# Kernel tuning notes

Hardware: AMD Instinct MI355X
Metric: run time of the kernel (lower is better)

Reference implementation:

```python
import jax, jax.numpy as jnp
import numpy as np

N_NODES = 100000
N_EDGES = 1600000
IN_FEATS = 64
OUT_FEATS = 64
DIM = 3
N_KERNELS = 4


def setup_inputs() -> dict:
    key = jax.random.key(0)
    ks = jax.random.split(key, 8)
    feat = jax.random.normal(ks[0], (N_NODES, IN_FEATS), dtype=jnp.float32)
    pseudo = jax.random.uniform(ks[1], (N_EDGES, DIM), dtype=jnp.float32)
    src = jax.random.randint(ks[2], (N_EDGES,), 0, N_NODES, dtype=jnp.int32)
    dst = jax.random.randint(ks[3], (N_EDGES,), 0, N_NODES, dtype=jnp.int32)
    W_fc = jax.random.normal(ks[4], (N_KERNELS * OUT_FEATS, IN_FEATS), dtype=jnp.float32) * 0.1
    mu = jax.random.normal(ks[5], (N_KERNELS, DIM), dtype=jnp.float32)
    inv_sigma = jax.random.uniform(ks[6], (N_KERNELS, DIM), dtype=jnp.float32) + 0.5
    bias = jnp.zeros((OUT_FEATS,), dtype=jnp.float32)
    return {"feat": feat, "pseudo": pseudo, "src": src, "dst": dst,
            "W_fc": W_fc, "mu": mu, "inv_sigma": inv_sigma, "bias": bias}


def reference(feat, pseudo, src, dst, W_fc, mu, inv_sigma, bias):
    N = feat.shape[0]
    K, out = N_KERNELS, OUT_FEATS
    # node projections: [N, K, out]
    h = (feat @ W_fc.T).reshape(N, K, out)
    # per-edge Gaussian kernel weights: [E, K]
    diff = pseudo[:, None, :] - mu[None, :, :]            # [E, K, dim]
    g = jnp.exp(jnp.sum(-0.5 * diff * diff * (inv_sigma[None] ** 2), axis=-1))
    # sum-aggregate: sum_k sum_{e: dst=v} h[src_e, k] * g[e, k]
    # (kernel sum and edge sum commute for sum reducer; loop over K avoids [E,K,out])
    rst = jnp.zeros((N, out), dtype=feat.dtype)
    for k in range(K):
        msg = h[:, k, :][src] * g[:, k:k + 1]             # [E, out]
        rst = rst + jax.ops.segment_sum(msg, dst, num_segments=N)
    # residual (Identity since in_feats == out_feats) + bias
    rst = rst + feat + bias
    return rst
```

## Files before the change

kernel.cpp:

```cpp
#include <hip/hip_runtime.h>

#define N_NODES_C 100000
#define N_EDGES_C 1600000
#define IN_F 64
#define OUT_F 64
#define NK 4
#define SCAN_BLK 256
#define NBLK ((N_NODES_C + SCAN_BLK - 1) / SCAN_BLK)
#define EBLK (N_EDGES_C / 256)
#define CPAD 16
#define NSLICE 8
#define SLICE_N (N_NODES_C / NSLICE)
#define SCAT_GRID 2048

__device__ __forceinline__ unsigned int f2bf(float x) {
    unsigned int u = __float_as_uint(x);
    return (u + 0x7fffu + ((u >> 16) & 1u)) >> 16;
}
__device__ __forceinline__ float bflo(unsigned int u) { return __uint_as_float(u << 16); }
__device__ __forceinline__ float bfhi(unsigned int u) { return __uint_as_float(u & 0xffff0000u); }

__global__ __launch_bounds__(256, 2) void proj_hist_kernel(
    const int* __restrict__ dst, int* __restrict__ cnt,
    const float* __restrict__ feat, const float* __restrict__ W,
    unsigned short* __restrict__ hb, int n_nodes)
{
    {
        const int gsz = (int)gridDim.x * 256;
        for (int e = (int)blockIdx.x * 256 + (int)threadIdx.x; e < N_EDGES_C; e += gsz)
            atomicAdd(&cnt[dst[e]], 1);
    }
    __shared__ float frow[4][IN_F];
    const int t = threadIdx.x;
    const int o = t >> 2;
    const int k = t & 3;
    float wreg[IN_F];
    {
        const float4* W4 = reinterpret_cast<const float4*>(W + (size_t)(k * OUT_F + o) * IN_F);
        #pragma unroll
        for (int i = 0; i < IN_F / 4; ++i) {
            float4 v = W4[i];
            wreg[4*i+0] = v.x; wreg[4*i+1] = v.y; wreg[4*i+2] = v.z; wreg[4*i+3] = v.w;
        }
    }
    const int nn4 = n_nodes >> 2;
    for (int q = blockIdx.x; q < nn4; q += gridDim.x) {
        const int n0 = q << 2;
        if (t < 64) {
            float4 v = reinterpret_cast<const float4*>(feat + (size_t)n0 * IN_F)[t];
            reinterpret_cast<float4*>(frow[t >> 4])[t & 15] = v;
        }
        __syncthreads();
        const float4* f0 = reinterpret_cast<const float4*>(frow[0]);
        const float4* f1 = reinterpret_cast<const float4*>(frow[1]);
        const float4* f2 = reinterpret_cast<const float4*>(frow[2]);
        const float4* f3 = reinterpret_cast<const float4*>(frow[3]);
        float a0 = 0.f, a1 = 0.f, a2 = 0.f, a3 = 0.f;
        #pragma unroll
        for (int i = 0; i < IN_F / 4; ++i) {
            const float4 v0 = f0[i], v1 = f1[i], v2 = f2[i], v3 = f3[i];
            const float w0 = wreg[4*i], w1 = wreg[4*i+1], w2 = wreg[4*i+2], w3 = wreg[4*i+3];
            a0 = fmaf(v0.x,w0, fmaf(v0.y,w1, fmaf(v0.z,w2, fmaf(v0.w,w3, a0))));
            a1 = fmaf(v1.x,w0, fmaf(v1.y,w1, fmaf(v1.z,w2, fmaf(v1.w,w3, a1))));
            a2 = fmaf(v2.x,w0, fmaf(v2.y,w1, fmaf(v2.z,w2, fmaf(v2.w,w3, a2))));
            a3 = fmaf(v3.x,w0, fmaf(v3.y,w1, fmaf(v3.z,w2, fmaf(v3.w,w3, a3))));
        }
        hb[(size_t)(n0+0) * 256 + t] = (unsigned short)f2bf(a0);
        hb[(size_t)(n0+1) * 256 + t] = (unsigned short)f2bf(a1);
        hb[(size_t)(n0+2) * 256 + t] = (unsigned short)f2bf(a2);
        hb[(size_t)(n0+3) * 256 + t] = (unsigned short)f2bf(a3);
        __syncthreads();
    }
}

__global__ __launch_bounds__(256) void scan1_kernel(
    const int* __restrict__ cnt, int* __restrict__ bsum)
{
    __shared__ int s[SCAN_BLK];
    int i = blockIdx.x * SCAN_BLK + threadIdx.x;
    int v = (i < N_NODES_C) ? cnt[i] : 0;
    s[threadIdx.x] = v; __syncthreads();
    for (int off = SCAN_BLK / 2; off > 0; off >>= 1) {
        if (threadIdx.x < off) s[threadIdx.x] += s[threadIdx.x + off];
        __syncthreads();
    }
    if (threadIdx.x == 0) bsum[blockIdx.x] = s[0];
}

__global__ __launch_bounds__(256) void scan23_kernel(
    const int* __restrict__ cnt, const int* __restrict__ bsum,
    int* __restrict__ row_start, int* __restrict__ cursor_pad)
{
    __shared__ int pre[SCAN_BLK];
    __shared__ int s[SCAN_BLK];
    const int t = threadIdx.x;
    int p = 0;
    for (int i = t; i < (int)blockIdx.x; i += SCAN_BLK) p += bsum[i];
    pre[t] = p; __syncthreads();
    for (int off = SCAN_BLK / 2; off > 0; off >>= 1) {
        if (t < off) pre[t] += pre[t + off];
        __syncthreads();
    }
    const int boff = pre[0];
    const int i = blockIdx.x * SCAN_BLK + t;
    int v = (i < N_NODES_C) ? cnt[i] : 0;
    s[t] = v; __syncthreads();
    for (int off = 1; off < SCAN_BLK; off <<= 1) {
        int x = (t >= off) ? s[t - off] : 0;
        __syncthreads();
        s[t] += x;
        __syncthreads();
    }
    if (i < N_NODES_C) {
        int ex = s[t] - v + boff;
        row_start[i] = ex;
        cursor_pad[(size_t)i * CPAD] = ex;
        if (i == N_NODES_C - 1) row_start[N_NODES_C] = ex + v;
    }
}

__global__ __launch_bounds__(256) void scatter_kernel(
    const int* __restrict__ src, const int* __restrict__ dst,
    const float* __restrict__ pseudo, const float* __restrict__ mu,
    const float* __restrict__ inv_sigma, int* __restrict__ cursor_pad,
    uint4* __restrict__ rec)
{
    float mm[NK*3], ss[NK*3];
    #pragma unroll
    for (int i = 0; i < NK*3; ++i) { mm[i] = mu[i]; ss[i] = inv_sigma[i]; }
    const int slice = (int)blockIdx.x & 7;
    const int w     = (int)blockIdx.x >> 3;
    const int lo = slice * SLICE_N, hi = lo + SLICE_N;
    for (int c = w; c < EBLK; c += SCAT_GRID / NSLICE) {
        const int e = c * 256 + (int)threadIdx.x;
        const int d = dst[e];
        if (d >= lo && d < hi) {
            const float p0 = pseudo[(size_t)e * 3 + 0];
            const float p1 = pseudo[(size_t)e * 3 + 1];
            const float p2 = pseudo[(size_t)e * 3 + 2];
            float g[NK];
            #pragma unroll
            for (int k = 0; k < NK; ++k) {
                const float d0 = p0 - mm[k*3+0], d1 = p1 - mm[k*3+1], d2 = p2 - mm[k*3+2];
                const float s0 = ss[k*3+0], s1 = ss[k*3+1], s2 = ss[k*3+2];
                g[k] = __expf(-0.5f * (d0*d0*s0*s0 + d1*d1*s1*s1 + d2*d2*s2*s2));
            }
            const int pos = atomicAdd(&cursor_pad[(size_t)d * CPAD], 1);
            uint4 r;
            r.x = (unsigned int)src[e];
            r.y = f2bf(g[0]) | (f2bf(g[1]) << 16);
            r.z = f2bf(g[2]) | (f2bf(g[3]) << 16);
            r.w = 0u;
            rec[pos] = r;
        }
    }
}

__global__ __launch_bounds__(256, 2) void gather_kernel(
    const int* __restrict__ row_start, const uint4* __restrict__ rec,
    const unsigned short* __restrict__ hb,
    const float* __restrict__ feat, const float* __restrict__ bias,
    float* __restrict__ out, int n_nodes)
{
    const int lane = threadIdx.x & 63;
    const int v = (blockIdx.x * 256 + threadIdx.x) >> 6;
    if (v >= n_nodes) return;
    const int r0 = row_start[v];
    const int r1 = row_start[v + 1];
    float acc = 0.f;
    int j = r0;
    const int jend4 = r0 + ((r1 - r0) & ~3);
    if (j < jend4) {
        uint4 a0 = rec[j+0], a1 = rec[j+1], a2 = rec[j+2], a3 = rec[j+3];
        j += 4;
        for (; j < jend4; j += 4) {
            const uint2 h0 = *(const uint2*)(hb + (size_t)a0.x * 256 + lane * 4);
            const uint2 h1 = *(const uint2*)(hb + (size_t)a1.x * 256 + lane * 4);
            const uint2 h2 = *(const uint2*)(hb + (size_t)a2.x * 256 + lane * 4);
            const uint2 h3 = *(const uint2*)(hb + (size_t)a3.x * 256 + lane * 4);
            const uint4 b0 = rec[j+0], b1 = rec[j+1], b2 = rec[j+2], b3 = rec[j+3];
            acc += bflo(a0.y)*bflo(h0.x) + bfhi(a0.y)*bfhi(h0.x)
                 + bflo(a0.z)*bflo(h0.y) + bfhi(a0.z)*bfhi(h0.y);
            acc += bflo(a1.y)*bflo(h1.x) + bfhi(a1.y)*bfhi(h1.x)
                 + bflo(a1.z)*bflo(h1.y) + bfhi(a1.z)*bfhi(h1.y);
            acc += bflo(a2.y)*bflo(h2.x) + bfhi(a2.y)*bfhi(h2.x)
                 + bflo(a2.z)*bflo(h2.y) + bfhi(a2.z)*bfhi(h2.y);
            acc += bflo(a3.y)*bflo(h3.x) + bfhi(a3.y)*bfhi(h3.x)
                 + bflo(a3.z)*bflo(h3.y) + bfhi(a3.z)*bfhi(h3.y);
            a0 = b0; a1 = b1; a2 = b2; a3 = b3;
        }
        {
            const uint2 h0 = *(const uint2*)(hb + (size_t)a0.x * 256 + lane * 4);
            const uint2 h1 = *(const uint2*)(hb + (size_t)a1.x * 256 + lane * 4);
            const uint2 h2 = *(const uint2*)(hb + (size_t)a2.x * 256 + lane * 4);
            const uint2 h3 = *(const uint2*)(hb + (size_t)a3.x * 256 + lane * 4);
            acc += bflo(a0.y)*bflo(h0.x) + bfhi(a0.y)*bfhi(h0.x)
                 + bflo(a0.z)*bflo(h0.y) + bfhi(a0.z)*bfhi(h0.y);
            acc += bflo(a1.y)*bflo(h1.x) + bfhi(a1.y)*bfhi(h1.x)
                 + bflo(a1.z)*bflo(h1.y) + bfhi(a1.z)*bfhi(h1.y);
            acc += bflo(a2.y)*bflo(h2.x) + bfhi(a2.y)*bfhi(h2.x)
                 + bflo(a2.z)*bflo(h2.y) + bfhi(a2.z)*bfhi(h2.y);
            acc += bflo(a3.y)*bflo(h3.x) + bfhi(a3.y)*bfhi(h3.x)
                 + bflo(a3.z)*bflo(h3.y) + bfhi(a3.z)*bfhi(h3.y);
        }
    }
    for (; j < r1; ++j) {
        const uint4 ra = rec[j];
        const uint2 ha = *(const uint2*)(hb + (size_t)ra.x * 256 + lane * 4);
        acc += bflo(ra.y)*bflo(ha.x) + bfhi(ra.y)*bfhi(ha.x)
             + bflo(ra.z)*bflo(ha.y) + bfhi(ra.z)*bfhi(ha.y);
    }
    out[(size_t)v * OUT_F + lane] = acc + feat[(size_t)v * OUT_F + lane] + bias[lane];
}

extern "C" void kernel_launch(void* const* d_in, const int* in_sizes, int n_in,
                              void* d_out, int out_size, void* d_ws, size_t ws_size,
                              hipStream_t stream) {
    const float* feat      = (const float*)d_in[0];
    const float* pseudo    = (const float*)d_in[1];
    const int*   src       = (const int*)d_in[2];
    const int*   dst       = (const int*)d_in[3];
    const float* W_fc      = (const float*)d_in[4];
    const float* mu        = (const float*)d_in[5];
    const float* inv_sigma = (const float*)d_in[6];
    const float* bias      = (const float*)d_in[7];
    float* out = (float*)d_out;

    char* ws = (char*)d_ws;
    unsigned short* hb = (unsigned short*)ws;  ws += (size_t)N_NODES_C * 256 * 2;
    uint4* rec         = (uint4*)ws;           ws += (size_t)N_EDGES_C * 16;
    int* cursor_pad    = (int*)ws;             ws += (size_t)N_NODES_C * CPAD * 4;
    int* cnt           = (int*)ws;             ws += (size_t)N_NODES_C * 4;
    int* row_start     = (int*)ws;             ws += (size_t)(N_NODES_C + 4) * 4;
    int* bsum          = (int*)ws;             ws += 512 * 4;

    hipMemsetAsync(cnt, 0, (size_t)N_NODES_C * 4, stream);
    proj_hist_kernel<<<SCAT_GRID, 256, 0, stream>>>(dst, cnt, feat, W_fc, hb, N_NODES_C);
    scan1_kernel<<<NBLK, SCAN_BLK, 0, stream>>>(cnt, bsum);
    scan23_kernel<<<NBLK, SCAN_BLK, 0, stream>>>(cnt, bsum, row_start, cursor_pad);
    scatter_kernel<<<SCAT_GRID, 256, 0, stream>>>(src, dst, pseudo, mu, inv_sigma,
                                                  cursor_pad, rec);
    gather_kernel<<<(N_NODES_C * 64 + 255) / 256, 256, 0, stream>>>(
        row_start, rec, hb, feat, bias, out, N_NODES_C);
}
```

Measured before the change: 321.0 us.

## Compute node projection with bf16 MFMA instead of scalar FMAs

Replaces the scalar fp32 register-tiled projection, which works on 4 nodes per iteration, with MFMA 16x16x32 bf16 instructions on 16-node tiles. W fragments are converted to bf16 once and kept in registers, and feat rows are loaded straight from global memory, which removes the shared-memory staging and the block barriers. Inputs are now rounded to bf16 before multiplication, so accuracy drops slightly. The projection is only one part of a kernel that also builds the edge histogram, and the other pipeline stages likely dominate total time.

```diff
diff --git a/kernel.cpp b/kernel.cpp
--- a/kernel.cpp
+++ b/kernel.cpp
@@ -13,12 +13,22 @@
 #define SLICE_N (N_NODES_C / NSLICE)
 #define SCAT_GRID 2048
 
+typedef __attribute__((ext_vector_type(8))) short bf16x8;
+typedef __attribute__((ext_vector_type(4))) float f32x4;
+
 __device__ __forceinline__ unsigned int f2bf(float x) {
     unsigned int u = __float_as_uint(x);
     return (u + 0x7fffu + ((u >> 16) & 1u)) >> 16;
 }
 __device__ __forceinline__ float bflo(unsigned int u) { return __uint_as_float(u << 16); }
 __device__ __forceinline__ float bfhi(unsigned int u) { return __uint_as_float(u & 0xffff0000u); }
+
+__device__ __forceinline__ bf16x8 cvt8(const float4 a, const float4 b) {
+    bf16x8 r;
+    r[0]=(short)f2bf(a.x); r[1]=(short)f2bf(a.y); r[2]=(short)f2bf(a.z); r[3]=(short)f2bf(a.w);
+    r[4]=(short)f2bf(b.x); r[5]=(short)f2bf(b.y); r[6]=(short)f2bf(b.z); r[7]=(short)f2bf(b.w);
+    return r;
+}
 
 __global__ __launch_bounds__(256, 2) void proj_hist_kernel(
     const int* __restrict__ dst, int* __restrict__ cnt,
@@ -30,46 +40,43 @@
         for (int e = (int)blockIdx.x * 256 + (int)threadIdx.x; e < N_EDGES_C; e += gsz)
             atomicAdd(&cnt[dst[e]], 1);
     }
-    __shared__ float frow[4][IN_F];
-    const int t = threadIdx.x;
-    const int o = t >> 2;
-    const int k = t & 3;
-    float wreg[IN_F];
-    {
-        const float4* W4 = reinterpret_cast<const float4*>(W + (size_t)(k * OUT_F + o) * IN_F);
+    const int t  = threadIdx.x;
+    const int wv = t >> 6;
+    const int l  = t & 63;
+    const int lr = l & 15;
+    const int lk = l >> 4;
+
+    bf16x8 bfrag[4][2];
+    #pragma unroll
+    for (int tile = 0; tile < 4; ++tile) {
+        const int col  = wv * 64 + tile * 16 + lr;
+        const int wrow = (col & 3) * 64 + (col >> 2);
         #pragma unroll
-        for (int i = 0; i < IN_F / 4; ++i) {
-            float4 v = W4[i];
-            wreg[4*i+0] = v.x; wreg[4*i+1] = v.y; wreg[4*i+2] = v.z; wreg[4*i+3] = v.w;
-        }
-    }
-    const int nn4 = n_nodes >> 2;
-    for (int q = blockIdx.x; q < nn4; q += gridDim.x) {
-        const int n0 = q << 2;
-        if (t < 64) {
-            float4 v = reinterpret_cast<const float4*>(feat + (size_t)n0 * IN_F)[t];
-            reinterpret_cast<float4*>(frow[t >> 4])[t & 15] = v;
-        }
-        __syncthreads();
-        const float4* f0 = reinterpret_cast<const float4*>(frow[0]);
-        const float4* f1 = reinterpret_cast<const float4*>(frow[1]);
-        const float4* f2 = reinterpret_cast<const float4*>(frow[2]);
-        const float4* f3 = reinterpret_cast<const float4*>(frow[3]);
-        float a0 = 0.f, a1 = 0.f, a2 = 0.f, a3 = 0.f;
+        for (int ks = 0; ks < 2; ++ks) {
+            const float4* wp = reinterpret_cast<const float4*>(
+                W + (size_t)wrow * IN_F + ks * 32 + lk * 8);
+            bfrag[tile][ks] = cvt8(wp[0], wp[1]);
+        }
+    }
+    const int ntile = n_nodes >> 4;
+    for (int q = blockIdx.x; q < ntile; q += gridDim.x) {
+        const int n0 = q << 4;
+        const float4* ap = reinterpret_cast<const float4*>(
+            feat + (size_t)(n0 + lr) * IN_F + lk * 8);
+        const float4* aq = reinterpret_cast<const float4*>(
+            feat + (size_t)(n0 + lr) * IN_F + 32 + lk * 8);
+        const bf16x8 a0 = cvt8(ap[0], ap[1]);
+        const bf16x8 a1 = cvt8(aq[0], aq[1]);
         #pragma unroll
-        for (int i = 0; i < IN_F / 4; ++i) {
-            const float4 v0 = f0[i], v1 = f1[i], v2 = f2[i], v3 = f3[i];
-            const float w0 = wreg[4*i], w1 = wreg[4*i+1], w2 = wreg[4*i+2], w3 = wreg[4*i+3];
-            a0 = fmaf(v0.x,w0, fmaf(v0.y,w1, fmaf(v0.z,w2, fmaf(v0.w,w3, a0))));
-            a1 = fmaf(v1.x,w0, fmaf(v1.y,w1, fmaf(v1.z,w2, fmaf(v1.w,w3, a1))));
-            a2 = fmaf(v2.x,w0, fmaf(v2.y,w1, fmaf(v2.z,w2, fmaf(v2.w,w3, a2))));
-            a3 = fmaf(v3.x,w0, fmaf(v3.y,w1, fmaf(v3.z,w2, fmaf(v3.w,w3, a3))));
-        }
-        hb[(size_t)(n0+0) * 256 + t] = (unsigned short)f2bf(a0);
-        hb[(size_t)(n0+1) * 256 + t] = (unsigned short)f2bf(a1);
-        hb[(size_t)(n0+2) * 256 + t] = (unsigned short)f2bf(a2);
-        hb[(size_t)(n0+3) * 256 + t] = (unsigned short)f2bf(a3);
-        __syncthreads();
+        for (int tile = 0; tile < 4; ++tile) {
+            f32x4 acc = {0.f, 0.f, 0.f, 0.f};
+            acc = __builtin_amdgcn_mfma_f32_16x16x32_bf16(a0, bfrag[tile][0], acc, 0, 0, 0);
+            acc = __builtin_amdgcn_mfma_f32_16x16x32_bf16(a1, bfrag[tile][1], acc, 0, 0, 0);
+            const int col = wv * 64 + tile * 16 + lr;
+            #pragma unroll
+            for (int r = 0; r < 4; ++r)
+                hb[(size_t)(n0 + lk * 4 + r) * 256 + col] = (unsigned short)f2bf(acc[r]);
+        }
     }
 }
 
```

Result: faster. 286.1 us (-10.9%).
